# Performance work log

Hardware: AMD Instinct MI355X
Metric: run time of the kernel (lower is better)

The kernel has to match this reference:

```python
import jax, jax.numpy as jnp
import numpy as np

N_NODES = 100000
NUM_FEATURES = 512
HIDDEN = 128
OUT = 2
N_EDGES = 1600000


def setup_inputs() -> dict:
    key = jax.random.key(0)
    k_x, k_e, k_w1, k_b1, k_w2, k_b2 = jax.random.split(key, 6)
    x = jax.random.normal(k_x, (N_NODES, NUM_FEATURES), dtype=jnp.float32)
    edge_index = jax.random.randint(k_e, (2, N_EDGES), 0, N_NODES, dtype=jnp.int64)
    # GCNConv weight (Glorot-style scale) and bias
    w1 = jax.random.normal(k_w1, (NUM_FEATURES, HIDDEN), dtype=jnp.float32) / np.sqrt(NUM_FEATURES)
    b1 = jnp.zeros((HIDDEN,), dtype=jnp.float32)
    # nn.Linear weight/bias
    w2 = jax.random.normal(k_w2, (HIDDEN, OUT), dtype=jnp.float32) / np.sqrt(HIDDEN)
    b2 = jnp.zeros((OUT,), dtype=jnp.float32)
    return {"x": x, "w1": w1, "b1": b1, "w2": w2, "b2": b2, "edge_index": edge_index}


def _gcn_conv(x, edge_index, w, b, num_nodes):
    """PyG GCNConv: h = D^{-1/2} (A+I) D^{-1/2} (x @ w) + b."""
    h = x @ w  # [N, hidden] -- transform before propagate (PyG order)
    loops = jnp.arange(num_nodes, dtype=edge_index.dtype)
    src = jnp.concatenate([edge_index[0], loops])  # [E+N]
    dst = jnp.concatenate([edge_index[1], loops])
    # symmetric normalization: deg computed over destination (col) incl. self-loops
    deg = jnp.zeros((num_nodes,), dtype=h.dtype).at[dst].add(1.0)
    dinv = jax.lax.rsqrt(deg)  # deg >= 1 thanks to self-loops
    norm = dinv[src] * dinv[dst]  # [E+N]
    msg = h[src] * norm[:, None]  # gather + scale, [E+N, hidden]
    out = jax.ops.segment_sum(msg, dst, num_segments=num_nodes)  # scatter-add
    return out + b


def reference(x, w1, b1, w2, b2, edge_index):
    h = _gcn_conv(x, edge_index, w1, b1, N_NODES)  # [N, hidden]
    return h @ w2 + b2  # [N, out]
```

## Files before the change

kernel.cpp:

```cpp
#include <hip/hip_runtime.h>

constexpr int N_NODES = 100000;
constexpr int N_FEAT  = 512;
constexpr int N_EDGES = 1600000;

constexpr float FXS = 1048576.0f;
constexpr float FXB = 32.0f;

constexpr int BSH   = 8;
constexpr int BINW  = 1 << BSH;
constexpr int NBINS = (N_NODES + BINW - 1) >> BSH;
constexpr int BCAP  = 5120;
constexpr int NBB   = 500;
constexpr int CHUNK = N_EDGES / NBB;
constexpr int NRB   = 1548;
constexpr int GRID  = NBB + NRB;

typedef float vfloat4 __attribute__((ext_vector_type(4)));

constexpr int WS_W    = 0;
constexpr int WS_C    = 1024;
constexpr int WS_CUR  = 1056;
constexpr int WS_DEG  = WS_CUR + 512;
constexpr int WS_DINV = WS_DEG + N_NODES;
constexpr int WS_G    = WS_DINV + N_NODES;
constexpr int WS_FXP  = WS_G + 2 * N_NODES;
constexpr int WS_BINS = WS_FXP + 2 * N_NODES;

static_assert((WS_FXP * 4) % 8 == 0, "fxp alignment");
static_assert(N_NODES % 4 == 0, "");

__global__ void k_prep(const float* __restrict__ w1, const float* __restrict__ w2,
                       const float* __restrict__ b1, const float* __restrict__ b2,
                       float* __restrict__ ws) {
    int i = blockIdx.x * blockDim.x + threadIdx.x;
    if (i < NBINS) reinterpret_cast<int*>(ws + WS_CUR)[i] = 0;
    if (i < N_FEAT) {
        float a0 = 0.f, a1 = 0.f;
        for (int m = 0; m < 128; ++m) {
            float w = w1[i * 128 + m];
            a0 += w * w2[m * 2 + 0];
            a1 += w * w2[m * 2 + 1];
        }
        ws[WS_W + i] = a0;
        ws[WS_W + 512 + i] = a1;
        if (i < 2) {
            float s = b2[i];
            for (int m = 0; m < 128; ++m) s += b1[m] * w2[m * 2 + i];
            ws[WS_C + i] = s;
        }
    }
}

__global__ __launch_bounds__(256) void k_fused(
    const float* __restrict__ x, float* __restrict__ ws,
    const int* __restrict__ src, const int* __restrict__ dst,
    float2* __restrict__ g) {
    int b = blockIdx.x;
    if (b < NBB) {
        __shared__ int cnt[NBINS];
        __shared__ int offs[NBINS];
        __shared__ int cur2[NBINS];
        int tid = threadIdx.x;
        for (int i = tid; i < NBINS; i += 256) { cnt[i] = 0; cur2[i] = 0; }
        __syncthreads();
        int base = b * CHUNK;
        for (int e = base + tid; e < base + CHUNK; e += 256)
            atomicAdd(&cnt[dst[e] >> BSH], 1);
        __syncthreads();
        int* gcur = reinterpret_cast<int*>(ws + WS_CUR);
        for (int i = tid; i < NBINS; i += 256) {
            int c = cnt[i];
            int pos = c ? atomicAdd(&gcur[i], c) : 0;
            offs[i] = i * BCAP + pos;
        }
        __syncthreads();
        unsigned int* bins = reinterpret_cast<unsigned int*>(ws + WS_BINS);
        for (int e = base + tid; e < base + CHUNK; e += 256) {
            int d = dst[e], s = src[e];
            int bin = d >> BSH;
            int r = atomicAdd(&cur2[bin], 1);
            bins[offs[bin] + r] = (unsigned int)s | ((unsigned int)(d & (BINW - 1)) << 17);
        }
        return;
    }
    int rb = b - NBB;
    const vfloat4* W0q = reinterpret_cast<const vfloat4*>(ws + WS_W);
    const vfloat4* W1q = reinterpret_cast<const vfloat4*>(ws + WS_W + 512);
    int lane = threadIdx.x & 63;
    int wave = threadIdx.x >> 6;
    int j = lane & 15, i4 = lane >> 4;

    vfloat4 w0[8], w1[8];
    #pragma unroll
    for (int k = 0; k < 8; ++k) {
        w0[k] = W0q[k * 16 + j];
        w1[k] = W1q[k * 16 + j];
    }

    int wid = rb * 4 + wave;
    int nw  = NRB * 4;
    constexpr int NQ = N_NODES / 4;
    for (int q = wid; q < NQ; q += nw) {
        int row = q * 4 + i4;
        const vfloat4* xr = reinterpret_cast<const vfloat4*>(x + (size_t)row * N_FEAT);
        vfloat4 xv[8];
        #pragma unroll
        for (int k = 0; k < 8; ++k)
            xv[k] = __builtin_nontemporal_load(&xr[k * 16 + j]);
        float a0 = 0.f, a1 = 0.f;
        #pragma unroll
        for (int k = 0; k < 8; ++k) {
            a0 += xv[k].x*w0[k].x + xv[k].y*w0[k].y + xv[k].z*w0[k].z + xv[k].w*w0[k].w;
            a1 += xv[k].x*w1[k].x + xv[k].y*w1[k].y + xv[k].z*w1[k].z + xv[k].w*w1[k].w;
        }
        #pragma unroll
        for (int off = 1; off <= 8; off <<= 1) {
            a0 += __shfl_xor(a0, off);
            a1 += __shfl_xor(a1, off);
        }
        if (j == 0) g[row] = make_float2(a0, a1);
    }
}

__global__ __launch_bounds__(256) void k_deg(float* __restrict__ ws) {
    int b = blockIdx.x;
    const int* gcur = reinterpret_cast<const int*>(ws + WS_CUR);
    const unsigned int* bins = reinterpret_cast<const unsigned int*>(ws + WS_BINS) + b * BCAP;
    int n = min(gcur[b], BCAP);
    __shared__ int cnt[BINW];
    cnt[threadIdx.x] = 0;
    __syncthreads();
    for (int i = threadIdx.x; i < n; i += 256)
        atomicAdd(&cnt[bins[i] >> 17], 1);
    __syncthreads();
    int d = (b << BSH) + threadIdx.x;
    if (d < N_NODES) {
        int dg = cnt[threadIdx.x] + 1;
        reinterpret_cast<int*>(ws + WS_DEG)[d] = dg;
        float di = rsqrtf((float)dg);
        ws[WS_DINV + d] = di;
        float2 gv = reinterpret_cast<const float2*>(ws + WS_G)[d];
        unsigned int lo = (unsigned int)__float2int_rn((gv.x * di + FXB) * FXS);
        unsigned int hi = (unsigned int)__float2int_rn((gv.y * di + FXB) * FXS);
        reinterpret_cast<unsigned long long*>(ws + WS_FXP)[d] =
            ((unsigned long long)hi << 32) | (unsigned long long)lo;
    }
}

__global__ __launch_bounds__(256) void k_pass2(float* __restrict__ ws,
                                               float2* __restrict__ out) {
    int b = blockIdx.x;
    const int* gcur = reinterpret_cast<const int*>(ws + WS_CUR);
    const unsigned int* bins = reinterpret_cast<const unsigned int*>(ws + WS_BINS) + b * BCAP;
    const int* deg = reinterpret_cast<const int*>(ws + WS_DEG);
    const float* dinv = ws + WS_DINV;
    const unsigned long long* fxp = reinterpret_cast<const unsigned long long*>(ws + WS_FXP);
    int n = min(gcur[b], BCAP);
    __shared__ unsigned long long acc[BINW];
    acc[threadIdx.x] = 0ull;
    __syncthreads();
    for (int i = threadIdx.x; i < n; i += 256) {
        unsigned int p = bins[i];
        atomicAdd(&acc[p >> 17], fxp[p & 0x1FFFFu]);
    }
    __syncthreads();
    int d = (b << BSH) + threadIdx.x;
    if (d < N_NODES) {
        unsigned long long a = acc[threadIdx.x] + fxp[d];
        long long dg = (long long)deg[d];
        long long bias = dg << 25;
        long long lo = (long long)(a & 0xFFFFFFFFull) - bias;
        long long hi = (long long)(a >> 32) - bias;
        float di = dinv[d];
        out[d] = make_float2(di * ((float)lo * (1.0f / FXS)) + ws[WS_C + 0],
                             di * ((float)hi * (1.0f / FXS)) + ws[WS_C + 1]);
    }
}

extern "C" void kernel_launch(void* const* d_in, const int* in_sizes, int n_in,
                              void* d_out, int out_size, void* d_ws, size_t ws_size,
                              hipStream_t stream) {
    const float* x  = (const float*)d_in[0];
    const float* w1 = (const float*)d_in[1];
    const float* b1 = (const float*)d_in[2];
    const float* w2 = (const float*)d_in[3];
    const float* b2 = (const float*)d_in[4];
    const int*   ei = (const int*)d_in[5];
    float* ws = (float*)d_ws;

    float2* g = (float2*)(ws + WS_G);

    k_prep<<<2, 256, 0, stream>>>(w1, w2, b1, b2, ws);
    k_fused<<<GRID, 256, 0, stream>>>(x, ws, ei, ei + N_EDGES, g);
    k_deg<<<NBINS, 256, 0, stream>>>(ws);
    k_pass2<<<NBINS, 256, 0, stream>>>(ws, (float2*)d_out);
}
```

Before: 86.21 us.

## Replace static row split with atomic work-stealing across all fused blocks

The GEMV row work was statically split over dedicated blocks, separate from the edge-binning blocks. Now every block, including the binning blocks once they finish, pulls 16-row chunks from 16 atomic dispatch counters kept in the workspace. This is meant to balance load between the binning and matvec phases so no blocks sit idle. The cost is extra global atomics per chunk and 16 more counters to zero in the prep kernel.

```diff
diff --git a/kernel.cpp b/kernel.cpp
--- a/kernel.cpp
+++ b/kernel.cpp
@@ -13,8 +13,12 @@
 constexpr int BCAP  = 5120;
 constexpr int NBB   = 500;
 constexpr int CHUNK = N_EDGES / NBB;
-constexpr int NRB   = 1548;
-constexpr int GRID  = NBB + NRB;
+constexpr int GRID  = 2048;
+
+constexpr int ROWCH  = 16;
+constexpr int NCHUNK = N_NODES / ROWCH;
+constexpr int NDISP  = 16;
+constexpr int RSZ    = (NCHUNK + NDISP - 1) / NDISP;
 
 typedef float vfloat4 __attribute__((ext_vector_type(4)));
 
@@ -28,13 +32,14 @@
 constexpr int WS_BINS = WS_FXP + 2 * N_NODES;
 
 static_assert((WS_FXP * 4) % 8 == 0, "fxp alignment");
-static_assert(N_NODES % 4 == 0, "");
+static_assert(N_NODES % ROWCH == 0, "");
+static_assert(NBINS + NDISP <= 512, "");
 
 __global__ void k_prep(const float* __restrict__ w1, const float* __restrict__ w2,
                        const float* __restrict__ b1, const float* __restrict__ b2,
                        float* __restrict__ ws) {
     int i = blockIdx.x * blockDim.x + threadIdx.x;
-    if (i < NBINS) reinterpret_cast<int*>(ws + WS_CUR)[i] = 0;
+    if (i < NBINS + NDISP) reinterpret_cast<int*>(ws + WS_CUR)[i] = 0;
     if (i < N_FEAT) {
         float a0 = 0.f, a1 = 0.f;
         for (int m = 0; m < 128; ++m) {
@@ -57,18 +62,19 @@
     const int* __restrict__ src, const int* __restrict__ dst,
     float2* __restrict__ g) {
     int b = blockIdx.x;
+    int tid = threadIdx.x;
+    int* gcur = reinterpret_cast<int*>(ws + WS_CUR);
+
     if (b < NBB) {
         __shared__ int cnt[NBINS];
         __shared__ int offs[NBINS];
         __shared__ int cur2[NBINS];
-        int tid = threadIdx.x;
         for (int i = tid; i < NBINS; i += 256) { cnt[i] = 0; cur2[i] = 0; }
         __syncthreads();
         int base = b * CHUNK;
         for (int e = base + tid; e < base + CHUNK; e += 256)
             atomicAdd(&cnt[dst[e] >> BSH], 1);
         __syncthreads();
-        int* gcur = reinterpret_cast<int*>(ws + WS_CUR);
         for (int i = tid; i < NBINS; i += 256) {
             int c = cnt[i];
             int pos = c ? atomicAdd(&gcur[i], c) : 0;
@@ -82,13 +88,12 @@
             int r = atomicAdd(&cur2[bin], 1);
             bins[offs[bin] + r] = (unsigned int)s | ((unsigned int)(d & (BINW - 1)) << 17);
         }
-        return;
-    }
-    int rb = b - NBB;
+    }
+
     const vfloat4* W0q = reinterpret_cast<const vfloat4*>(ws + WS_W);
     const vfloat4* W1q = reinterpret_cast<const vfloat4*>(ws + WS_W + 512);
-    int lane = threadIdx.x & 63;
-    int wave = threadIdx.x >> 6;
+    int lane = tid & 63;
+    int wave = tid >> 6;
     int j = lane & 15, i4 = lane >> 4;
 
     vfloat4 w0[8], w1[8];
@@ -98,28 +103,45 @@
         w1[k] = W1q[k * 16 + j];
     }
 
-    int wid = rb * 4 + wave;
-    int nw  = NRB * 4;
-    constexpr int NQ = N_NODES / 4;
-    for (int q = wid; q < NQ; q += nw) {
-        int row = q * 4 + i4;
-        const vfloat4* xr = reinterpret_cast<const vfloat4*>(x + (size_t)row * N_FEAT);
-        vfloat4 xv[8];
-        #pragma unroll
-        for (int k = 0; k < 8; ++k)
-            xv[k] = __builtin_nontemporal_load(&xr[k * 16 + j]);
-        float a0 = 0.f, a1 = 0.f;
-        #pragma unroll
-        for (int k = 0; k < 8; ++k) {
-            a0 += xv[k].x*w0[k].x + xv[k].y*w0[k].y + xv[k].z*w0[k].z + xv[k].w*w0[k].w;
-            a1 += xv[k].x*w1[k].x + xv[k].y*w1[k].y + xv[k].z*w1[k].z + xv[k].w*w1[k].w;
-        }
-        #pragma unroll
-        for (int off = 1; off <= 8; off <<= 1) {
-            a0 += __shfl_xor(a0, off);
-            a1 += __shfl_xor(a1, off);
-        }
-        if (j == 0) g[row] = make_float2(a0, a1);
+    int* disp = gcur + NBINS;
+    int d0 = (b * 4 + wave) & (NDISP - 1);
+    for (int t = 0; t < NDISP; ++t) {
+        int d = (d0 + t) & (NDISP - 1);
+        int rbase = d * RSZ;
+        int rend  = min(rbase + RSZ, NCHUNK);
+        int seen = 0;
+        if (lane == 0)
+            seen = __hip_atomic_load(&disp[d], __ATOMIC_RELAXED, __HIP_MEMORY_SCOPE_AGENT);
+        seen = __shfl(seen, 0);
+        if (rbase + seen >= rend) continue;
+        while (true) {
+            int c = 0;
+            if (lane == 0) c = atomicAdd(&disp[d], 1);
+            c = __shfl(c, 0);
+            int chunk = rbase + c;
+            if (chunk >= rend) break;
+            #pragma unroll
+            for (int it = 0; it < 4; ++it) {
+                int row = chunk * ROWCH + it * 4 + i4;
+                const vfloat4* xr = reinterpret_cast<const vfloat4*>(x + (size_t)row * N_FEAT);
+                vfloat4 xv[8];
+                #pragma unroll
+                for (int k = 0; k < 8; ++k)
+                    xv[k] = __builtin_nontemporal_load(&xr[k * 16 + j]);
+                float a0 = 0.f, a1 = 0.f;
+                #pragma unroll
+                for (int k = 0; k < 8; ++k) {
+                    a0 += xv[k].x*w0[k].x + xv[k].y*w0[k].y + xv[k].z*w0[k].z + xv[k].w*w0[k].w;
+                    a1 += xv[k].x*w1[k].x + xv[k].y*w1[k].y + xv[k].z*w1[k].z + xv[k].w*w1[k].w;
+                }
+                #pragma unroll
+                for (int off = 1; off <= 8; off <<= 1) {
+                    a0 += __shfl_xor(a0, off);
+                    a1 += __shfl_xor(a1, off);
+                }
+                if (j == 0) g[row] = make_float2(a0, a1);
+            }
+        }
     }
 }
 
```

Measured after the change: 285.5 us. 231% more time.
